# Optimization experiments

Measured on AMD Instinct MI355X. Metric: run time of the kernel, lower is better.

## Reference

```python
import jax, jax.numpy as jnp
import numpy as np

N = 100000   # nodes
E = 1600000  # edges
G = 256      # graphs in batch
F_IN = 64
H = 64
C = 10


def setup_inputs() -> dict:
    key = jax.random.key(0)
    ks = jax.random.split(key, 16)
    x = jax.random.normal(ks[0], (N, F_IN), dtype=jnp.float32)
    edge_index = jax.random.randint(ks[1], (2, E), 0, N, dtype=jnp.int32)
    batch = jnp.sort(jax.random.randint(ks[2], (N,), 0, G, dtype=jnp.int32))
    def lin(k, i, o):
        return jax.random.normal(k, (i, o), dtype=jnp.float32) / np.sqrt(i).astype(np.float32)
    return {
        'x': x, 'edge_index': edge_index, 'batch': batch,
        'W1': lin(ks[3], F_IN, H), 'b1': jnp.zeros((H,), jnp.float32),
        'W2': lin(ks[4], H, H),    'b2': jnp.zeros((H,), jnp.float32),
        'W3': lin(ks[5], H, H),    'b3': jnp.zeros((H,), jnp.float32),
        'fc1_w': lin(ks[6], 3 * H, H),      'fc1_b': jnp.zeros((H,), jnp.float32),
        'fc2_w': lin(ks[7], H, H // 2),     'fc2_b': jnp.zeros((H // 2,), jnp.float32),
        'fc3_w': lin(ks[8], H // 2, C),     'fc3_b': jnp.zeros((C,), jnp.float32),
    }


def _gcn_layer(h_in, W, b, src, dst, deg_inv_sqrt):
    # GCNConv: h = X W ; out = D^-1/2 (A + I) D^-1/2 h + b ; then ReLU
    h = h_in @ W
    norm = deg_inv_sqrt[src] * deg_inv_sqrt[dst]            # [E]
    agg = jax.ops.segment_sum(h[src] * norm[:, None], dst, num_segments=N)
    agg = agg + h * (deg_inv_sqrt * deg_inv_sqrt)[:, None]  # self-loop term
    return jax.nn.relu(agg + b)


def _pool(h, batch):
    # concat(mean, max, add) pooling by graph id
    s = jax.ops.segment_sum(h, batch, num_segments=G)
    cnt = jax.ops.segment_sum(jnp.ones((h.shape[0], 1), h.dtype), batch, num_segments=G)
    mean = s / jnp.maximum(cnt, 1.0)
    mx = jnp.maximum(jax.ops.segment_max(h, batch, num_segments=G), 0.0)  # h >= 0 post-ReLU
    return jnp.concatenate([mean, mx, s], axis=1)  # [G, 3H]


def reference(x, edge_index, batch, W1, b1, W2, b2, W3, b3,
              fc1_w, fc1_b, fc2_w, fc2_b, fc3_w, fc3_b):
    src, dst = edge_index[0], edge_index[1]
    # degree including self loop (edge weight 1)
    deg = jax.ops.segment_sum(jnp.ones((E,), x.dtype), dst, num_segments=N) + 1.0
    dis = jax.lax.rsqrt(deg)

    h1 = _gcn_layer(x, W1, b1, src, dst, dis)
    p1 = _pool(h1, batch)
    h2 = _gcn_layer(h1, W2, b2, src, dst, dis)
    p2 = _pool(h2, batch)
    h3 = _gcn_layer(h2, W3, b3, src, dst, dis)
    p3 = _pool(h3, batch)

    z = p1 + p2 + p3                              # [G, 3H]
    z = jax.nn.relu(z @ fc1_w + fc1_b)            # dropout inactive (eval)
    z = jax.nn.relu(z @ fc2_w + fc2_b)
    return jax.nn.log_softmax(z @ fc3_w + fc3_b, axis=-1)
```

## Files before the change

### kernel.cpp

```cpp
#include <hip/hip_runtime.h>
#include <cmath>

typedef unsigned int uint;
typedef __attribute__((ext_vector_type(8))) short short8;
typedef __attribute__((ext_vector_type(4))) float f32x4;
typedef __attribute__((ext_vector_type(4))) int i32x4;

__device__ inline float bflo(uint u) { return __uint_as_float(u << 16); }
__device__ inline float bfhi(uint u) { return __uint_as_float(u & 0xffff0000u); }
__device__ inline ushort bf1(float a) {
  uint ua = __float_as_uint(a);
  return (ushort)((ua + 0x7fffu + ((ua >> 16) & 1u)) >> 16);
}
__device__ inline uint bfpack(float a, float b) {
  uint ua = __float_as_uint(a), ub = __float_as_uint(b);
  uint ra = (ua + 0x7fffu + ((ua >> 16) & 1u)) >> 16;
  uint rb = (ub + 0x7fffu + ((ub >> 16) & 1u)) >> 16;
  return ra | (rb << 16);
}

#define SLOT_CAP 48
#define FILL_CHUNK 4096
#define BSHIFT 8
#define NPB 256
#define MAXB 512
#define BCAP 5120

__global__ __launch_bounds__(256) void prep_k(const float* __restrict__ W1, const float* __restrict__ W2,
                                              const float* __restrict__ W3,
                                              ushort* __restrict__ T1, ushort* __restrict__ T2,
                                              ushort* __restrict__ T3,
                                              const int* __restrict__ batch, int* __restrict__ gstart,
                                              int* __restrict__ bcnt, ushort* __restrict__ sbuf,
                                              float* __restrict__ zpool, int zcount,
                                              int n, int G, int bnd) {
  int b = blockIdx.x;
  int t = threadIdx.x;
  if (b < 48) {
    int sel = b >> 4;
    int i = (b & 15) * 256 + t;
    const float* W = (sel == 0) ? W1 : (sel == 1) ? W2 : W3;
    ushort* T = (sel == 0) ? T1 : (sel == 1) ? T2 : T3;
    int c = i >> 6, k = i & 63;
    T[i] = bf1(W[k * 64 + c]);
  } else if (b < 48 + bnd) {
    int i = (b - 48) * 256 + t;
    if (i >= n) return;
    int bb = batch[i];
    int prev = (i == 0) ? -1 : batch[i - 1];
    for (int g = prev + 1; g <= bb; ++g) gstart[g] = i;
    if (i == n - 1) { for (int g = bb + 1; g <= G; ++g) gstart[g] = n; }
  } else if (b == 48 + bnd) {
    if (t < 32) ((uint*)(sbuf + (size_t)n * 64))[t] = 0u;
    bcnt[t] = 0; bcnt[t + 256] = 0;
  } else {
    int idx = (b - 49 - bnd) * 256 + t;
    if (idx < zcount) zpool[idx] = 0.f;
  }
}

__global__ __launch_bounds__(256) void part_k(const int* __restrict__ src, const int* __restrict__ dst,
                                              int* __restrict__ bcnt, uint* __restrict__ buckets,
                                              int E, int nb) {
  __shared__ int lcnt[MAXB], lbase[MAXB];
  int t = threadIdx.x;
  for (int i = t; i < nb; i += 256) lcnt[i] = 0;
  __syncthreads();
  int base = blockIdx.x * FILL_CHUNK;
  int d[16];
  #pragma unroll
  for (int i = 0; i < 16; ++i) {
    int e = base + t + i * 256;
    d[i] = (e < E) ? __builtin_nontemporal_load(dst + e) : -1;
    if (d[i] >= 0) atomicAdd(&lcnt[d[i] >> BSHIFT], 1);
  }
  __syncthreads();
  for (int i = t; i < nb; i += 256) { lbase[i] = atomicAdd(&bcnt[i], lcnt[i]); lcnt[i] = 0; }
  __syncthreads();
  #pragma unroll
  for (int i = 0; i < 16; ++i) {
    if (d[i] >= 0) {
      int e = base + t + i * 256;
      int r = d[i] >> BSHIFT;
      int rank = atomicAdd(&lcnt[r], 1);
      uint s = (uint)__builtin_nontemporal_load(src + e);
      uint packed = (s << 8) | (uint)(d[i] & (NPB - 1));
      buckets[(size_t)r * BCAP + lbase[r] + rank] = packed;
    }
  }
}

__global__ __launch_bounds__(256) void fillB_k(const uint* __restrict__ buckets,
                                               const int* __restrict__ bcnt,
                                               int* __restrict__ cursor, int* __restrict__ csr,
                                               float* __restrict__ dis,
                                               int nb, int N) {
  __shared__ int lcnt[NPB];
  __shared__ int rows[NPB][SLOT_CAP];
  int r = blockIdx.x;
  int t = threadIdx.x;
  if (t < NPB) lcnt[t] = 0;
  i32x4* rinit = (i32x4*)&rows[0][0];
  for (int i = t; i < NPB * SLOT_CAP / 4; i += 256) rinit[i] = (i32x4){N, N, N, N};
  __syncthreads();
  int n = bcnt[r];
  const uint* bk = buckets + (size_t)r * BCAP;
  for (int i = t; i < n; i += 256) {
    uint e = __builtin_nontemporal_load(&bk[i]);
    int dl = (int)(e & (NPB - 1));
    int s = (int)(e >> 8);
    int pos = atomicAdd(&lcnt[dl], 1);
    if (pos < SLOT_CAP) rows[dl][pos] = s;
  }
  __syncthreads();
  int base_node = r << BSHIFT;
  int nodes_here = N - base_node; if (nodes_here > NPB) nodes_here = NPB;
  if (nodes_here <= 0) return;
  int total4 = nodes_here * (SLOT_CAP / 4);
  i32x4* dstp = (i32x4*)(csr + (size_t)base_node * SLOT_CAP);
  const i32x4* srcp = (const i32x4*)&rows[0][0];
  for (int i = t; i < total4; i += 256) dstp[i] = srcp[i];
  for (int i = t; i < nodes_here; i += 256) {
    int c = lcnt[i];
    cursor[base_node + i] = c;
    dis[base_node + i] = rsqrtf((float)c + 1.0f);
  }
}

__global__ __launch_bounds__(256) void xcast_k(const float* __restrict__ X, const float* __restrict__ dis,
                                               ushort* __restrict__ S, int total4) {
  int i = blockIdx.x * 256 + threadIdx.x;
  if (i >= total4) return;
  float ds = dis[i >> 4];
  float4 v = ((const float4*)X)[i];
  ((uint2*)S)[i] = make_uint2(bfpack(v.x * ds, v.y * ds), bfpack(v.z * ds, v.w * ds));
}

__global__ __launch_bounds__(256) void agg_k(const ushort* __restrict__ S,
                                             const int* __restrict__ csr,
                                             const int* __restrict__ cnt,
                                             const float* __restrict__ dis,
                                             ushort* __restrict__ P, int n) {
  int wv = __builtin_amdgcn_readfirstlane((int)(threadIdx.x >> 6));
  int lane = threadIdx.x & 63;
  int node = blockIdx.x * 4 + wv;
  if (node >= n) return;
  float dn = dis[node];
  int deg = __builtin_nontemporal_load(cnt + node);
  if (deg > SLOT_CAP) deg = SLOT_CAP;
  const i32x4* rp = (const i32x4*)(csr + (size_t)node * SLOT_CAP);
  float acc = bflo((uint)S[(size_t)node * 64 + lane]);

  i32x4 r0 = __builtin_nontemporal_load(rp + 0);
  i32x4 r1 = __builtin_nontemporal_load(rp + 1);
  i32x4 r2 = __builtin_nontemporal_load(rp + 2);
  i32x4 r3 = __builtin_nontemporal_load(rp + 3);
  i32x4 r4 = __builtin_nontemporal_load(rp + 4);
  i32x4 r5 = __builtin_nontemporal_load(rp + 5);
  i32x4 r6 = __builtin_nontemporal_load(rp + 6);
  i32x4 r7 = __builtin_nontemporal_load(rp + 7);
  int sa[32] = {r0.x, r0.y, r0.z, r0.w, r1.x, r1.y, r1.z, r1.w,
                r2.x, r2.y, r2.z, r2.w, r3.x, r3.y, r3.z, r3.w,
                r4.x, r4.y, r4.z, r4.w, r5.x, r5.y, r5.z, r5.w,
                r6.x, r6.y, r6.z, r6.w, r7.x, r7.y, r7.z, r7.w};
  float ha[32];
  #pragma unroll
  for (int i = 0; i < 32; ++i) ha[i] = bflo((uint)S[(size_t)sa[i] * 64 + lane]);
  #pragma unroll
  for (int i = 0; i < 32; ++i) acc += ha[i];

  if (deg > 32) {
    i32x4 r8  = __builtin_nontemporal_load(rp + 8);
    i32x4 r9  = __builtin_nontemporal_load(rp + 9);
    i32x4 r10 = __builtin_nontemporal_load(rp + 10);
    i32x4 r11 = __builtin_nontemporal_load(rp + 11);
    int sb[16] = {r8.x, r8.y, r8.z, r8.w, r9.x, r9.y, r9.z, r9.w,
                  r10.x, r10.y, r10.z, r10.w, r11.x, r11.y, r11.z, r11.w};
    float hb[16];
    #pragma unroll
    for (int i = 0; i < 16; ++i) hb[i] = bflo((uint)S[(size_t)sb[i] * 64 + lane]);
    #pragma unroll
    for (int i = 0; i < 16; ++i) acc += hb[i];
  }

  P[(size_t)node * 64 + lane] = bf1(dn * acc);
}

__global__ __launch_bounds__(256) void gemmP_k(const ushort* __restrict__ P,
                                               const ushort* __restrict__ WT,
                                               const float* __restrict__ dis,
                                               const float* __restrict__ bias,
                                               const int* __restrict__ batch,
                                               ushort* __restrict__ Sout,
                                               float* __restrict__ zsum, uint* __restrict__ zmax,
                                               int n) {
  int t = threadIdx.x;
  int wv = t >> 6, lane = t & 63;
  int m = lane & 15, quad = lane >> 4;
  int row = blockIdx.x * 64 + wv * 16 + m;
  int rclamp = (row < n) ? row : 0;
  const short8* arow = (const short8*)(P + (size_t)rclamp * 64);
  short8 a0 = arow[quad];
  short8 a1 = arow[quad + 4];
  f32x4 acc[4];
  #pragma unroll
  for (int ct = 0; ct < 4; ++ct) {
    const short8* wrow = (const short8*)(WT + (size_t)(ct * 16 + m) * 64);
    short8 b0 = wrow[quad];
    short8 b1 = wrow[quad + 4];
    f32x4 a = {0.f, 0.f, 0.f, 0.f};
    a = __builtin_amdgcn_mfma_f32_16x16x32_bf16(a0, b0, a, 0, 0, 0);
    a = __builtin_amdgcn_mfma_f32_16x16x32_bf16(a1, b1, a, 0, 0, 0);
    acc[ct] = a;
  }
  int blockRow = blockIdx.x * 64;
  int g0 = batch[blockRow];
  int rl = blockRow + 63; if (rl > n - 1) rl = n - 1;
  int gl = batch[rl];
  int orow = blockRow + wv * 16 + quad * 4;
  float s0a[4] = {0.f, 0.f, 0.f, 0.f}, s1a[4] = {0.f, 0.f, 0.f, 0.f};
  float m0a[4] = {0.f, 0.f, 0.f, 0.f}, m1a[4] = {0.f, 0.f, 0.f, 0.f};
  #pragma unroll
  for (int reg = 0; reg < 4; ++reg) {
    int r = orow + reg;
    bool valid = (r < n);
    int gr = valid ? batch[r] : g0;
    bool to1 = (gr != g0);
    float ds = valid ? dis[r] : 0.f;
    #pragma unroll
    for (int ct = 0; ct < 4; ++ct) {
      float h = valid ? fmaxf(acc[ct][reg] + bias[ct * 16 + m], 0.f) : 0.f;
      if (Sout && valid) Sout[(size_t)r * 64 + ct * 16 + m] = bf1(h * ds);
      if (to1) { s1a[ct] += h; m1a[ct] = fmaxf(m1a[ct], h); }
      else     { s0a[ct] += h; m0a[ct] = fmaxf(m0a[ct], h); }
    }
  }
  #pragma unroll
  for (int msk = 16; msk <= 32; msk <<= 1) {
    #pragma unroll
    for (int ct = 0; ct < 4; ++ct) {
      s0a[ct] += __shfl_xor(s0a[ct], msk, 64);
      s1a[ct] += __shfl_xor(s1a[ct], msk, 64);
      m0a[ct] = fmaxf(m0a[ct], __shfl_xor(m0a[ct], msk, 64));
      m1a[ct] = fmaxf(m1a[ct], __shfl_xor(m1a[ct], msk, 64));
    }
  }
  __shared__ float ls0[4][64], ls1[4][64], lm0[4][64], lm1[4][64];
  if (quad == 0) {
    #pragma unroll
    for (int ct = 0; ct < 4; ++ct) {
      ls0[wv][ct * 16 + m] = s0a[ct]; ls1[wv][ct * 16 + m] = s1a[ct];
      lm0[wv][ct * 16 + m] = m0a[ct]; lm1[wv][ct * 16 + m] = m1a[ct];
    }
  }
  __syncthreads();
  if (t < 64) {
    float S0 = (ls0[0][t] + ls0[1][t]) + (ls0[2][t] + ls0[3][t]);
    float M0 = fmaxf(fmaxf(lm0[0][t], lm0[1][t]), fmaxf(lm0[2][t], lm0[3][t]));
    atomicAdd(&zsum[g0 * 64 + t], S0);
    atomicMax(&zmax[g0 * 64 + t], __float_as_uint(M0));
    if (gl != g0) {
      float S1 = (ls1[0][t] + ls1[1][t]) + (ls1[2][t] + ls1[3][t]);
      float M1 = fmaxf(fmaxf(lm1[0][t], lm1[1][t]), fmaxf(lm1[2][t], lm1[3][t]));
      atomicAdd(&zsum[gl * 64 + t], S1);
      atomicMax(&zmax[gl * 64 + t], __float_as_uint(M1));
    }
  }
}

__global__ __launch_bounds__(64) void mlp_k(const float* __restrict__ zsum,
                                            const uint* __restrict__ zmax, int G64,
                                            const int* __restrict__ gstart,
                                            const float* __restrict__ fc1w, const float* __restrict__ fc1b,
                                            const float* __restrict__ fc2w, const float* __restrict__ fc2b,
                                            const float* __restrict__ fc3w, const float* __restrict__ fc3b,
                                            float* __restrict__ out) {
  int g = blockIdx.x; int t = threadIdx.x;
  __shared__ float zr[192], a1[64], a2[32], a3[10];
  float S = zsum[g * 64 + t];
  float M = __uint_as_float(zmax[g * 64 + t])
          + __uint_as_float(zmax[G64 + g * 64 + t])
          + __uint_as_float(zmax[2 * G64 + g * 64 + t]);
  float cntf = (float)(gstart[g + 1] - gstart[g]);
  zr[t]       = (cntf > 0.f) ? S / cntf : 0.f;
  zr[64 + t]  = M;
  zr[128 + t] = S;
  __syncthreads();
  float acc = fc1b[t];
  for (int k = 0; k < 192; ++k) acc += zr[k] * fc1w[k * 64 + t];
  a1[t] = fmaxf(acc, 0.f);
  __syncthreads();
  if (t < 32) {
    float a = fc2b[t];
    #pragma unroll
    for (int k = 0; k < 64; ++k) a += a1[k] * fc2w[k * 32 + t];
    a2[t] = fmaxf(a, 0.f);
  }
  __syncthreads();
  if (t < 10) {
    float a = fc3b[t];
    #pragma unroll
    for (int k = 0; k < 32; ++k) a += a2[k] * fc3w[k * 10 + t];
    a3[t] = a;
  }
  __syncthreads();
  if (t == 0) {
    float mx = a3[0];
    for (int i = 1; i < 10; ++i) mx = fmaxf(mx, a3[i]);
    float sum = 0.f;
    for (int i = 0; i < 10; ++i) sum += expf(a3[i] - mx);
    float lse = mx + logf(sum);
    for (int i = 0; i < 10; ++i) out[g * 10 + i] = a3[i] - lse;
  }
}

extern "C" void kernel_launch(void* const* d_in, const int* in_sizes, int n_in,
                              void* d_out, int out_size, void* d_ws, size_t ws_size,
                              hipStream_t stream) {
  const float* x    = (const float*)d_in[0];
  const int*   ei   = (const int*)  d_in[1];
  const int*   batch= (const int*)  d_in[2];
  const float* W1   = (const float*)d_in[3];
  const float* b1   = (const float*)d_in[4];
  const float* W2   = (const float*)d_in[5];
  const float* b2   = (const float*)d_in[6];
  const float* W3   = (const float*)d_in[7];
  const float* b3   = (const float*)d_in[8];
  const float* fc1w = (const float*)d_in[9];
  const float* fc1b = (const float*)d_in[10];
  const float* fc2w = (const float*)d_in[11];
  const float* fc2b = (const float*)d_in[12];
  const float* fc3w = (const float*)d_in[13];
  const float* fc3b = (const float*)d_in[14];
  float* out = (float*)d_out;

  const int N = in_sizes[0] / 64;
  const int E = in_sizes[1] / 2;
  const int G = out_size / 10;
  const int* src = ei;
  const int* dst = ei + E;
  const int nb = (N + NPB - 1) >> BSHIFT;

  char* p = (char*)d_ws;
  auto alloc = [&](size_t bytes) -> void* {
    void* r = (void*)p; p += (bytes + 255) & ~(size_t)255; return r;
  };
  int*       cursor  = (int*)      alloc((size_t)N * 4);
  int*       bcnt    = (int*)      alloc(MAXB * 4);
  float*     dis     = (float*)    alloc((size_t)N * 4);
  int*       gstart  = (int*)      alloc((size_t)(G + 1) * 4);
  int*       csr     = (int*)      alloc((size_t)(nb * NPB) * SLOT_CAP * 4);
  uint*      buckets = (uint*)     alloc((size_t)nb * BCAP * 4);
  ushort*    wt1     = (ushort*)   alloc(4096 * 2);
  ushort*    wt2     = (ushort*)   alloc(4096 * 2);
  ushort*    wt3     = (ushort*)   alloc(4096 * 2);
  ushort*    sbuf    = (ushort*)   alloc((size_t)(N + 1) * 64 * 2);
  ushort*    pbuf    = (ushort*)   alloc((size_t)N * 64 * 2);
  float*     zpool   = (float*)    alloc((size_t)4 * G * 64 * 4);
  float*     zsum    = zpool;
  uint*      zmax    = (uint*)(zpool + (size_t)G * 64);
  (void)ws_size; (void)n_in;

  int G64 = G * 64;
  int bnd = (N + 255) >> 8;
  int zcount = 4 * G64;
  int prep_grid = 48 + bnd + 1 + (zcount + 255) / 256;
  prep_k<<<prep_grid, 256, 0, stream>>>(W1, W2, W3, wt1, wt2, wt3, batch, gstart,
                                        bcnt, sbuf, zpool, zcount, N, G, bnd);
  int chunks = (E + FILL_CHUNK - 1) / FILL_CHUNK;
  part_k<<<chunks, 256, 0, stream>>>(src, dst, bcnt, buckets, E, nb);
  fillB_k<<<nb, 256, 0, stream>>>(buckets, bcnt, cursor, csr, dis, nb, N);
  xcast_k<<<(N * 16 + 255) / 256, 256, 0, stream>>>(x, dis, sbuf, N * 16);

  int gb = (N + 63) / 64;
  int ab = (N + 3) / 4;
  agg_k<<<ab, 256, 0, stream>>>(sbuf, csr, cursor, dis, pbuf, N);
  gemmP_k<<<gb, 256, 0, stream>>>(pbuf, wt1, dis, b1, batch, sbuf, zsum, zmax + 0 * G64, N);
  agg_k<<<ab, 256, 0, stream>>>(sbuf, csr, cursor, dis, pbuf, N);
  gemmP_k<<<gb, 256, 0, stream>>>(pbuf, wt2, dis, b2, batch, sbuf, zsum, zmax + 1 * G64, N);
  agg_k<<<ab, 256, 0, stream>>>(sbuf, csr, cursor, dis, pbuf, N);
  gemmP_k<<<gb, 256, 0, stream>>>(pbuf, wt3, dis, b3, batch, nullptr, zsum, zmax + 2 * G64, N);

  mlp_k<<<G, 64, 0, stream>>>(zsum, zmax, G64, gstart, fc1w, fc1b, fc2w, fc2b, fc3w, fc3b, out);
}
```

Measured before the change: 299.7 us.

## Fuse aggregation with GEMM per layer and fold x cast into CSR fill

Each GCN layer's gather-aggregate and MFMA GEMM/pool are merged into one kernel. Each wave aggregates 16 nodes, stages the bf16 rows in swizzled LDS and feeds them straight to the MFMA, which removes the P buffer round-trip through global memory and one launch per layer. Ping-pong S buffers replace in-place reuse, since fused layers cannot overwrite their input. The x-to-bf16 scaled cast also moves into fillB_k. Each wave now processes 16 nodes sequentially, which may reduce memory-level parallelism compared with one node per wave across many more blocks.

Result: slower. 392.7 us (+31.0%).

```diff
diff --git a/kernel.cpp b/kernel.cpp
--- a/kernel.cpp
+++ b/kernel.cpp
@@ -94,6 +94,7 @@
                                                const int* __restrict__ bcnt,
                                                int* __restrict__ cursor, int* __restrict__ csr,
                                                float* __restrict__ dis,
+                                               const float* __restrict__ X, ushort* __restrict__ Sb,
                                                int nb, int N) {
   __shared__ int lcnt[NPB];
   __shared__ int rows[NPB][SLOT_CAP];
@@ -125,70 +126,20 @@
     cursor[base_node + i] = c;
     dis[base_node + i] = rsqrtf((float)c + 1.0f);
   }
-}
-
-__global__ __launch_bounds__(256) void xcast_k(const float* __restrict__ X, const float* __restrict__ dis,
-                                               ushort* __restrict__ S, int total4) {
-  int i = blockIdx.x * 256 + threadIdx.x;
-  if (i >= total4) return;
-  float ds = dis[i >> 4];
-  float4 v = ((const float4*)X)[i];
-  ((uint2*)S)[i] = make_uint2(bfpack(v.x * ds, v.y * ds), bfpack(v.z * ds, v.w * ds));
-}
-
-__global__ __launch_bounds__(256) void agg_k(const ushort* __restrict__ S,
-                                             const int* __restrict__ csr,
-                                             const int* __restrict__ cnt,
-                                             const float* __restrict__ dis,
-                                             ushort* __restrict__ P, int n) {
-  int wv = __builtin_amdgcn_readfirstlane((int)(threadIdx.x >> 6));
-  int lane = threadIdx.x & 63;
-  int node = blockIdx.x * 4 + wv;
-  if (node >= n) return;
-  float dn = dis[node];
-  int deg = __builtin_nontemporal_load(cnt + node);
-  if (deg > SLOT_CAP) deg = SLOT_CAP;
-  const i32x4* rp = (const i32x4*)(csr + (size_t)node * SLOT_CAP);
-  float acc = bflo((uint)S[(size_t)node * 64 + lane]);
-
-  i32x4 r0 = __builtin_nontemporal_load(rp + 0);
-  i32x4 r1 = __builtin_nontemporal_load(rp + 1);
-  i32x4 r2 = __builtin_nontemporal_load(rp + 2);
-  i32x4 r3 = __builtin_nontemporal_load(rp + 3);
-  i32x4 r4 = __builtin_nontemporal_load(rp + 4);
-  i32x4 r5 = __builtin_nontemporal_load(rp + 5);
-  i32x4 r6 = __builtin_nontemporal_load(rp + 6);
-  i32x4 r7 = __builtin_nontemporal_load(rp + 7);
-  int sa[32] = {r0.x, r0.y, r0.z, r0.w, r1.x, r1.y, r1.z, r1.w,
-                r2.x, r2.y, r2.z, r2.w, r3.x, r3.y, r3.z, r3.w,
-                r4.x, r4.y, r4.z, r4.w, r5.x, r5.y, r5.z, r5.w,
-                r6.x, r6.y, r6.z, r6.w, r7.x, r7.y, r7.z, r7.w};
-  float ha[32];
-  #pragma unroll
-  for (int i = 0; i < 32; ++i) ha[i] = bflo((uint)S[(size_t)sa[i] * 64 + lane]);
-  #pragma unroll
-  for (int i = 0; i < 32; ++i) acc += ha[i];
-
-  if (deg > 32) {
-    i32x4 r8  = __builtin_nontemporal_load(rp + 8);
-    i32x4 r9  = __builtin_nontemporal_load(rp + 9);
-    i32x4 r10 = __builtin_nontemporal_load(rp + 10);
-    i32x4 r11 = __builtin_nontemporal_load(rp + 11);
-    int sb[16] = {r8.x, r8.y, r8.z, r8.w, r9.x, r9.y, r9.z, r9.w,
-                  r10.x, r10.y, r10.z, r10.w, r11.x, r11.y, r11.z, r11.w};
-    float hb[16];
-    #pragma unroll
-    for (int i = 0; i < 16; ++i) hb[i] = bflo((uint)S[(size_t)sb[i] * 64 + lane]);
-    #pragma unroll
-    for (int i = 0; i < 16; ++i) acc += hb[i];
-  }
-
-  P[(size_t)node * 64 + lane] = bf1(dn * acc);
-}
-
-__global__ __launch_bounds__(256) void gemmP_k(const ushort* __restrict__ P,
+  for (int i = t; i < nodes_here * 16; i += 256) {
+    int nl = i >> 4, c4 = i & 15;
+    float ds = rsqrtf((float)lcnt[nl] + 1.0f);
+    float4 v = ((const float4*)(X + ((size_t)(base_node + nl) << 6)))[c4];
+    ((uint2*)(Sb + ((size_t)(base_node + nl) << 6)))[c4] =
+        make_uint2(bfpack(v.x * ds, v.y * ds), bfpack(v.z * ds, v.w * ds));
+  }
+}
+
+__global__ __launch_bounds__(256) void layer_k(const ushort* __restrict__ S,
+                                               const int* __restrict__ csr,
+                                               const int* __restrict__ cnt,
+                                               const float* __restrict__ dis,
                                                const ushort* __restrict__ WT,
-                                               const float* __restrict__ dis,
                                                const float* __restrict__ bias,
                                                const int* __restrict__ batch,
                                                ushort* __restrict__ Sout,
@@ -196,12 +147,57 @@
                                                int n) {
   int t = threadIdx.x;
   int wv = t >> 6, lane = t & 63;
+  __shared__ __align__(16) ushort plds[4][16 * 64];
+  ushort* wl = plds[wv];
+  int base = blockIdx.x * 64 + wv * 16;
+
+  for (int i = 0; i < 16; ++i) {
+    int node = base + i;
+    float pval = 0.f;
+    if (node < n) {
+      float dn = dis[node];
+      int deg = __builtin_nontemporal_load(cnt + node);
+      if (deg > SLOT_CAP) deg = SLOT_CAP;
+      const i32x4* rp = (const i32x4*)(csr + (size_t)node * SLOT_CAP);
+      float acc = bflo((uint)S[(size_t)node * 64 + lane]);
+      i32x4 r0 = __builtin_nontemporal_load(rp + 0);
+      i32x4 r1 = __builtin_nontemporal_load(rp + 1);
+      i32x4 r2 = __builtin_nontemporal_load(rp + 2);
+      i32x4 r3 = __builtin_nontemporal_load(rp + 3);
+      i32x4 r4 = __builtin_nontemporal_load(rp + 4);
+      i32x4 r5 = __builtin_nontemporal_load(rp + 5);
+      i32x4 r6 = __builtin_nontemporal_load(rp + 6);
+      i32x4 r7 = __builtin_nontemporal_load(rp + 7);
+      int sa[32] = {r0.x, r0.y, r0.z, r0.w, r1.x, r1.y, r1.z, r1.w,
+                    r2.x, r2.y, r2.z, r2.w, r3.x, r3.y, r3.z, r3.w,
+                    r4.x, r4.y, r4.z, r4.w, r5.x, r5.y, r5.z, r5.w,
+                    r6.x, r6.y, r6.z, r6.w, r7.x, r7.y, r7.z, r7.w};
+      float ha[32];
+      #pragma unroll
+      for (int j = 0; j < 32; ++j) ha[j] = bflo((uint)S[(size_t)sa[j] * 64 + lane]);
+      #pragma unroll
+      for (int j = 0; j < 32; ++j) acc += ha[j];
+      if (deg > 32) {
+        i32x4 r8  = __builtin_nontemporal_load(rp + 8);
+        i32x4 r9  = __builtin_nontemporal_load(rp + 9);
+        i32x4 r10 = __builtin_nontemporal_load(rp + 10);
+        i32x4 r11 = __builtin_nontemporal_load(rp + 11);
+        int sb[16] = {r8.x, r8.y, r8.z, r8.w, r9.x, r9.y, r9.z, r9.w,
+                      r10.x, r10.y, r10.z, r10.w, r11.x, r11.y, r11.z, r11.w};
+        float hb[16];
+        #pragma unroll
+        for (int j = 0; j < 16; ++j) hb[j] = bflo((uint)S[(size_t)sb[j] * 64 + lane]);
+        #pragma unroll
+        for (int j = 0; j < 16; ++j) acc += hb[j];
+      }
+      pval = dn * acc;
+    }
+    wl[(i << 6) + ((((lane >> 3) ^ (i & 7)) << 3)) + (lane & 7)] = bf1(pval);
+  }
+
   int m = lane & 15, quad = lane >> 4;
-  int row = blockIdx.x * 64 + wv * 16 + m;
-  int rclamp = (row < n) ? row : 0;
-  const short8* arow = (const short8*)(P + (size_t)rclamp * 64);
-  short8 a0 = arow[quad];
-  short8 a1 = arow[quad + 4];
+  short8 a0 = *(const short8*)&wl[(m << 6) + (((quad     ^ (m & 7)) << 3))];
+  short8 a1 = *(const short8*)&wl[(m << 6) + ((((quad+4) ^ (m & 7)) << 3))];
   f32x4 acc[4];
   #pragma unroll
   for (int ct = 0; ct < 4; ++ct) {
@@ -355,7 +351,7 @@
   ushort*    wt2     = (ushort*)   alloc(4096 * 2);
   ushort*    wt3     = (ushort*)   alloc(4096 * 2);
   ushort*    sbuf    = (ushort*)   alloc((size_t)(N + 1) * 64 * 2);
-  ushort*    pbuf    = (ushort*)   alloc((size_t)N * 64 * 2);
+  ushort*    sbuf2   = (ushort*)   alloc((size_t)(N + 1) * 64 * 2);
   float*     zpool   = (float*)    alloc((size_t)4 * G * 64 * 4);
   float*     zsum    = zpool;
   uint*      zmax    = (uint*)(zpool + (size_t)G * 64);
@@ -367,19 +363,15 @@
   int prep_grid = 48 + bnd + 1 + (zcount + 255) / 256;
   prep_k<<<prep_grid, 256, 0, stream>>>(W1, W2, W3, wt1, wt2, wt3, batch, gstart,
                                         bcnt, sbuf, zpool, zcount, N, G, bnd);
+  (void)hipMemsetAsync(sbuf2 + (size_t)N * 64, 0, 64 * 2, stream);
   int chunks = (E + FILL_CHUNK - 1) / FILL_CHUNK;
   part_k<<<chunks, 256, 0, stream>>>(src, dst, bcnt, buckets, E, nb);
-  fillB_k<<<nb, 256, 0, stream>>>(buckets, bcnt, cursor, csr, dis, nb, N);
-  xcast_k<<<(N * 16 + 255) / 256, 256, 0, stream>>>(x, dis, sbuf, N * 16);
+  fillB_k<<<nb, 256, 0, stream>>>(buckets, bcnt, cursor, csr, dis, x, sbuf, nb, N);
 
   int gb = (N + 63) / 64;
-  int ab = (N + 3) / 4;
-  agg_k<<<ab, 256, 0, stream>>>(sbuf, csr, cursor, dis, pbuf, N);
-  gemmP_k<<<gb, 256, 0, stream>>>(pbuf, wt1, dis, b1, batch, sbuf, zsum, zmax + 0 * G64, N);
-  agg_k<<<ab, 256, 0, stream>>>(sbuf, csr, cursor, dis, pbuf, N);
-  gemmP_k<<<gb, 256, 0, stream>>>(pbuf, wt2, dis, b2, batch, sbuf, zsum, zmax + 1 * G64, N);
-  agg_k<<<ab, 256, 0, stream>>>(sbuf, csr, cursor, dis, pbuf, N);
-  gemmP_k<<<gb, 256, 0, stream>>>(pbuf, wt3, dis, b3, batch, nullptr, zsum, zmax + 2 * G64, N);
+  layer_k<<<gb, 256, 0, stream>>>(sbuf, csr, cursor, dis, wt1, b1, batch, sbuf2, zsum, zmax + 0 * G64, N);
+  layer_k<<<gb, 256, 0, stream>>>(sbuf2, csr, cursor, dis, wt2, b2, batch, sbuf, zsum, zmax + 1 * G64, N);
+  layer_k<<<gb, 256, 0, stream>>>(sbuf, csr, cursor, dis, wt3, b3, batch, nullptr, zsum, zmax + 2 * G64, N);
 
   mlp_k<<<G, 64, 0, stream>>>(zsum, zmax, G64, gstart, fc1w, fc1b, fc2w, fc2b, fc3w, fc3b, out);
 }
```
